# Kernel tuning notes

Measured on AMD Instinct MI355X. Metric: run time of the kernel, lower is better.

## Reference

```python
import jax, jax.numpy as jnp
import numpy as np

NUM_BINS = 256
HIST_MIN = -1.0
HIST_MAX = 1.0
EPS = 1e-8


def _histc(x, bins=NUM_BINS, lo=HIST_MIN, hi=HIST_MAX):
    # Faithful to torch.histc: values outside [lo, hi] are ignored;
    # value == hi falls into the last bin.
    x = x.reshape(-1)
    width = (hi - lo) / bins
    idx = jnp.clip(jnp.floor((x - lo) / width).astype(jnp.int32), 0, bins - 1)
    in_range = ((x >= lo) & (x <= hi)).astype(jnp.float32)
    return jax.ops.segment_sum(in_range, idx, num_segments=bins)


def _entropy(hist):
    prob = hist / jnp.sum(hist) + EPS
    return -jnp.sum(prob * jnp.log(prob))


def setup_inputs() -> dict:
    key = jax.random.key(0)
    k1, k2 = jax.random.split(key)
    shape = (64, 2, 512, 512)
    predicted_ab = jax.random.normal(k1, shape, dtype=jnp.float32)
    ground_truth_ab = jax.random.normal(k2, shape, dtype=jnp.float32)
    return {"predicted_ab": predicted_ab, "ground_truth_ab": ground_truth_ab}


def reference(predicted_ab, ground_truth_ab):
    pred_hist = _histc(predicted_ab)
    gt_hist = _histc(ground_truth_ab)
    return jnp.abs(_entropy(pred_hist) - _entropy(gt_hist))
```

## Files before the change

### kernel.cpp

```cpp
#include <hip/hip_runtime.h>
#include <math.h>

#define NBINS 256
#define NCOPY 32


__device__ __forceinline__ void proc4(float4 v, unsigned int* __restrict__ lh, int c) {
    float vv[4] = {v.x, v.y, v.z, v.w};
#pragma unroll
    for (int j = 0; j < 4; j++) {
        float f = vv[j];
        if (f >= -1.0f && f <= 1.0f) {
            int bin = (int)((f + 1.0f) * 128.0f);
            bin = bin > (NBINS - 1) ? (NBINS - 1) : bin;
            atomicAdd(&lh[(bin << 5) + c], 1u);
        }
    }
}

__global__ __launch_bounds__(256) void hist2_kernel(const float* __restrict__ a,
                                                    const float* __restrict__ b,
                                                    unsigned int* __restrict__ ghist,
                                                    int n4a, int n4b, int half_blocks) {
    __shared__ unsigned int lh[NBINS * NCOPY];
    const int tid = threadIdx.x;
    for (int i = tid; i < NBINS * NCOPY; i += 256) lh[i] = 0u;
    __syncthreads();

    const int which = (blockIdx.x >= half_blocks) ? 1 : 0;
    const float4* __restrict__ x4 = (const float4*)(which ? b : a);
    const int n4 = which ? n4b : n4a;
    const int bid = which ? (blockIdx.x - half_blocks) : blockIdx.x;
    const int c = tid & (NCOPY - 1);

    const int chunk = (n4 + half_blocks - 1) / half_blocks;
    const int beg = bid * chunk;
    const int end = (beg + chunk < n4) ? (beg + chunk) : n4;

    int i = beg + tid;
    for (; i + 3 * 256 < end; i += 4 * 256) {
        float4 v0 = x4[i];
        float4 v1 = x4[i + 256];
        float4 v2 = x4[i + 512];
        float4 v3 = x4[i + 768];
        __builtin_amdgcn_sched_barrier(0);
        proc4(v0, lh, c);
        proc4(v1, lh, c);
        proc4(v2, lh, c);
        proc4(v3, lh, c);
    }
    for (; i < end; i += 256) {
        proc4(x4[i], lh, c);
    }
    __syncthreads();

    unsigned int s = 0;
#pragma unroll
    for (int k = 0; k < NCOPY; k++) s += lh[(tid << 5) + ((k + tid) & (NCOPY - 1))];
    atomicAdd(&ghist[which * NBINS + tid], s);
}

__global__ __launch_bounds__(256) void entropy_kernel(const unsigned int* __restrict__ gh,
                                                      float* __restrict__ out) {
    __shared__ double sd[NBINS];
    const int tid = threadIdx.x;
    double e[2];

    for (int h = 0; h < 2; h++) {
        const double hv = (double)gh[h * NBINS + tid];

        sd[tid] = hv;
        __syncthreads();
        for (int o = 128; o > 0; o >>= 1) {
            if (tid < o) sd[tid] += sd[tid + o];
            __syncthreads();
        }
        const double total = sd[0];
        __syncthreads();

        const double p = hv / total + 1e-8;
        sd[tid] = -p * log(p);
        __syncthreads();
        for (int o = 128; o > 0; o >>= 1) {
            if (tid < o) sd[tid] += sd[tid + o];
            __syncthreads();
        }
        e[h] = sd[0];
        __syncthreads();
    }

    if (tid == 0) out[0] = (float)fabs(e[0] - e[1]);
}

extern "C" void kernel_launch(void* const* d_in, const int* in_sizes, int n_in,
                              void* d_out, int out_size, void* d_ws, size_t ws_size,
                              hipStream_t stream) {
    const float* pred = (const float*)d_in[0];
    const float* gt   = (const float*)d_in[1];
    const int n0 = in_sizes[0];
    const int n1 = in_sizes[1];

    unsigned int* hist = (unsigned int*)d_ws;
    hipMemsetAsync(d_ws, 0, 2 * NBINS * sizeof(unsigned int), stream);

    const int half_blocks = 512;
    hist2_kernel<<<2 * half_blocks, 256, 0, stream>>>(pred, gt, hist,
                                                      n0 / 4, n1 / 4, half_blocks);
    entropy_kernel<<<1, 256, 0, stream>>>(hist, (float*)d_out);
}
```

Baseline: 282.5 us.

## Replace shared-memory atomics with per-thread private 16-bit histograms

New measurement: 327.7 us. 16.0% more time.

```diff
diff --git a/kernel.cpp b/kernel.cpp
--- a/kernel.cpp
+++ b/kernel.cpp
@@ -2,62 +2,83 @@
 #include <math.h>
 
 #define NBINS 256
-#define NCOPY 32
+#define TPB 128
 
 
-__device__ __forceinline__ void proc4(float4 v, unsigned int* __restrict__ lh, int c) {
+__device__ __forceinline__ void procgrp(float4 v, unsigned short* __restrict__ lh,
+                                        int tid) {
     float vv[4] = {v.x, v.y, v.z, v.w};
+    int bn[4], val[4], idx[4];
 #pragma unroll
     for (int j = 0; j < 4; j++) {
         float f = vv[j];
-        if (f >= -1.0f && f <= 1.0f) {
-            int bin = (int)((f + 1.0f) * 128.0f);
-            bin = bin > (NBINS - 1) ? (NBINS - 1) : bin;
-            atomicAdd(&lh[(bin << 5) + c], 1u);
-        }
+        int ok = (f >= -1.0f) & (f <= 1.0f);
+        int bb = (int)((f + 1.0f) * 128.0f);
+        bb = bb > (NBINS - 1) ? (NBINS - 1) : bb;
+        bn[j] = ok ? bb : 0;
+        val[j] = ok;
+        idx[j] = (bn[j] << 7) + tid;
     }
+    unsigned short r0 = lh[idx[0]];
+    unsigned short r1 = lh[idx[1]];
+    unsigned short r2 = lh[idx[2]];
+    unsigned short r3 = lh[idx[3]];
+    int inc0 = val[0];
+    int inc1 = val[1] + ((bn[0] == bn[1]) & val[0]);
+    int inc2 = val[2] + ((bn[0] == bn[2]) & val[0]) + ((bn[1] == bn[2]) & val[1]);
+    int inc3 = val[3] + ((bn[0] == bn[3]) & val[0]) + ((bn[1] == bn[3]) & val[1])
+                      + ((bn[2] == bn[3]) & val[2]);
+    lh[idx[0]] = (unsigned short)(r0 + inc0);
+    lh[idx[1]] = (unsigned short)(r1 + inc1);
+    lh[idx[2]] = (unsigned short)(r2 + inc2);
+    lh[idx[3]] = (unsigned short)(r3 + inc3);
 }
 
-__global__ __launch_bounds__(256) void hist2_kernel(const float* __restrict__ a,
+__global__ __launch_bounds__(TPB) void hist2_kernel(const float* __restrict__ a,
                                                     const float* __restrict__ b,
                                                     unsigned int* __restrict__ ghist,
                                                     int n4a, int n4b, int half_blocks) {
-    __shared__ unsigned int lh[NBINS * NCOPY];
+    __shared__ unsigned short lh[NBINS * TPB];
     const int tid = threadIdx.x;
-    for (int i = tid; i < NBINS * NCOPY; i += 256) lh[i] = 0u;
+
+    {
+        uint4* p = (uint4*)lh;
+#pragma unroll
+        for (int k = 0; k < 32; k++) p[k * TPB + tid] = make_uint4(0u, 0u, 0u, 0u);
+    }
     __syncthreads();
 
     const int which = (blockIdx.x >= half_blocks) ? 1 : 0;
     const float4* __restrict__ x4 = (const float4*)(which ? b : a);
     const int n4 = which ? n4b : n4a;
     const int bid = which ? (blockIdx.x - half_blocks) : blockIdx.x;
-    const int c = tid & (NCOPY - 1);
 
     const int chunk = (n4 + half_blocks - 1) / half_blocks;
     const int beg = bid * chunk;
     const int end = (beg + chunk < n4) ? (beg + chunk) : n4;
 
     int i = beg + tid;
-    for (; i + 3 * 256 < end; i += 4 * 256) {
+    for (; i + TPB < end; i += 2 * TPB) {
         float4 v0 = x4[i];
-        float4 v1 = x4[i + 256];
-        float4 v2 = x4[i + 512];
-        float4 v3 = x4[i + 768];
-        __builtin_amdgcn_sched_barrier(0);
-        proc4(v0, lh, c);
-        proc4(v1, lh, c);
-        proc4(v2, lh, c);
-        proc4(v3, lh, c);
+        float4 v1 = x4[i + TPB];
+        procgrp(v0, lh, tid);
+        procgrp(v1, lh, tid);
     }
-    for (; i < end; i += 256) {
-        proc4(x4[i], lh, c);
-    }
+    for (; i < end; i += TPB) procgrp(x4[i], lh, tid);
     __syncthreads();
 
-    unsigned int s = 0;
+    const unsigned int* l32 = (const unsigned int*)lh;
 #pragma unroll
-    for (int k = 0; k < NCOPY; k++) s += lh[(tid << 5) + ((k + tid) & (NCOPY - 1))];
-    atomicAdd(&ghist[which * NBINS + tid], s);
+    for (int half = 0; half < 2; half++) {
+        const int bin = tid + half * TPB;
+        unsigned int s = 0;
+#pragma unroll 8
+        for (int j = 0; j < 64; j++) {
+            unsigned int w = l32[(bin << 6) + ((j + tid) & 63)];
+            s += (w & 0xFFFFu) + (w >> 16);
+        }
+        atomicAdd(&ghist[which * NBINS + bin], s);
+    }
 }
 
 __global__ __launch_bounds__(256) void entropy_kernel(const unsigned int* __restrict__ gh,
@@ -104,7 +125,7 @@
     hipMemsetAsync(d_ws, 0, 2 * NBINS * sizeof(unsigned int), stream);
 
     const int half_blocks = 512;
-    hist2_kernel<<<2 * half_blocks, 256, 0, stream>>>(pred, gt, hist,
+    hist2_kernel<<<2 * half_blocks, TPB, 0, stream>>>(pred, gt, hist,
                                                       n0 / 4, n1 / 4, half_blocks);
     entropy_kernel<<<1, 256, 0, stream>>>(hist, (float*)d_out);
 }
```
